# Kernel tuning notes

Measured on AMD Instinct MI355X. Metric: run time of the kernel, lower is better.

The kernel has to match this reference:

```python
import jax, jax.numpy as jnp
import numpy as np

TOP_K = 8
N_GROUPS = 8
TOP_K_GROUPS = 4
ROUTE_SCALE = 2.5


def setup_inputs() -> dict:
    key = jax.random.key(0)
    k1, k2, k3 = jax.random.split(key, 3)
    x = jax.random.normal(k1, (8192, 7168), dtype=jnp.float32)
    weight = jax.random.normal(k2, (256, 7168), dtype=jnp.float32) * 0.02
    bias = jax.random.normal(k3, (256,), dtype=jnp.float32) * 0.1
    return {"x": x, "weight": weight, "bias": bias}


def reference(x, weight, bias):
    n_tokens = x.shape[0]
    n_experts = weight.shape[0]
    # scores: [T, E]
    logits = jnp.einsum('td,ed->te', x, weight)
    scores = jax.nn.sigmoid(logits)
    original_scores = scores
    scores_b = scores + bias  # bias branch (dim == 7168)
    # group-limited routing
    sg = scores_b.reshape(n_tokens, N_GROUPS, n_experts // N_GROUPS)
    # bias is not None -> group score = sum of top-2 within group
    top2, _ = jax.lax.top_k(sg, 2)
    group_scores = top2.sum(axis=-1)  # [T, G]
    _, group_idx = jax.lax.top_k(group_scores, TOP_K_GROUPS)  # [T, Kg]
    keep = jnp.zeros((n_tokens, N_GROUPS), dtype=bool)
    keep = keep.at[jnp.arange(n_tokens)[:, None], group_idx].set(True)
    masked = jnp.where(keep[:, :, None], sg, -jnp.inf).reshape(n_tokens, n_experts)
    # global top-k over masked scores
    _, indices = jax.lax.top_k(masked, TOP_K)  # [T, K]
    weights = jnp.take_along_axis(original_scores, indices, axis=1)
    weights = weights / weights.sum(axis=-1, keepdims=True)  # sigmoid normalization
    weights = weights * ROUTE_SCALE
    return weights.astype(x.dtype), indices
```

## Files before the change

### kernel.cpp

```cpp
#include <hip/hip_runtime.h>
#include <math.h>

#define T_TOKENS 8192
#define NEXP 256
#define DIM 7168
#define NEG_INF (-3.0e38f)

typedef _Float16 f16;
typedef _Float16 f16x8 __attribute__((ext_vector_type(8)));
typedef __fp16 h16x2 __attribute__((ext_vector_type(2)));
typedef float f32x4 __attribute__((ext_vector_type(4)));

#define AS1 __attribute__((address_space(1)))
#define AS3 __attribute__((address_space(3)))

#define WTILED_BYTES (2 * NEXP * DIM * 2)
#define PART_OFF WTILED_BYTES
#define UNSCALE 5.9604644775390625e-8f

__global__ __launch_bounds__(256) void wconvert(const float* __restrict__ w,
                                                char* __restrict__ wt) {
    const int n = blockIdx.x * 256 + threadIdx.x;
    const int K8 = n % 896;
    const int e = n / 896;
    const f32x4 u0 = *(const f32x4*)(w + (size_t)e * DIM + K8 * 8);
    const f32x4 u1 = *(const f32x4*)(w + (size_t)e * DIM + K8 * 8 + 4);
    float c[8] = {u0[0]*4096.f, u0[1]*4096.f, u0[2]*4096.f, u0[3]*4096.f,
                  u1[0]*4096.f, u1[1]*4096.f, u1[2]*4096.f, u1[3]*4096.f};
    f16x8 h, g;
#pragma unroll
    for (int j = 0; j < 4; ++j) {
        h16x2 hp = __builtin_amdgcn_cvt_pkrtz(c[2*j], c[2*j+1]);
        float r0 = c[2*j]   - (float)hp[0];
        float r1 = c[2*j+1] - (float)hp[1];
        h16x2 gp = __builtin_amdgcn_cvt_pkrtz(r0, r1);
        h[2*j] = (f16)hp[0]; h[2*j+1] = (f16)hp[1];
        g[2*j] = (f16)gp[0]; g[2*j+1] = (f16)gp[1];
    }
    const int T = K8 >> 2, q = K8 & 3;
    const int bnq = e >> 6, nt = (e >> 4) & 3, l = e & 15;
    char* base = wt + ((size_t)(T * 4 + bnq)) * 8192 + q * 256 + l * 16;
    *(f16x8*)(base + (0 * 4 + nt) * 1024) = h;
    *(f16x8*)(base + (1 * 4 + nt) * 1024) = g;
}

__global__ __launch_bounds__(512) void gemm8w(
    const float* __restrict__ x, const char* __restrict__ wt,
    float* __restrict__ part, int ksplit) {
    __shared__ char smem[65536];
    const int tid = threadIdx.x;
    const int lane = tid & 63;
    const int wv = tid >> 6;
    const int bn = blockIdx.x, bm = blockIdx.y, bz = blockIdx.z;
    const int wr = wv >> 2, wcn = wv & 3;
    const int l15 = lane & 15, q4 = lane >> 4;
    const int niter = ksplit >> 5;

    const char* xc = (const char*)x;

    int aoff[2], ldsA[2];
#pragma unroll
    for (int i = 0; i < 2; ++i) {
        const int u = wv * 2 + i;
        const int ra = u * 8 + (lane >> 3);
        const int ua = lane & 7;
        aoff[i] = (bm * 128 + ra) * (DIM * 4) + bz * (ksplit * 4)
                + ((ua ^ (ra & 7)) * 16);
        ldsA[i] = u * 1024;
    }
    const char* wbase0 = wt + ((size_t)(bz * niter * 4 + bn * 2)) * 8192;
    int woff[2], ldsW[2];
#pragma unroll
    for (int i = 0; i < 2; ++i) {
        const int u = wv * 2 + i;
        woff[i] = u * 1024 + lane * 16;
        ldsW[i] = 16384 + u * 1024;
    }

    int rA[4][2];
#pragma unroll
    for (int m = 0; m < 4; ++m) {
        const int r = wr * 64 + m * 16 + l15;
        rA[m][0] = r * 128 + (((2 * q4 + 0) ^ (r & 7)) * 16);
        rA[m][1] = r * 128 + (((2 * q4 + 1) ^ (r & 7)) * 16);
    }
    int rW[2][2];
#pragma unroll
    for (int ntl = 0; ntl < 2; ++ntl)
#pragma unroll
        for (int p = 0; p < 2; ++p)
            rW[ntl][p] = 16384 + (wcn >> 1) * 8192
                       + (p * 4 + (wcn & 1) * 2 + ntl) * 1024 + q4 * 256 + l15 * 16;

    f32x4 acc[4][2];
#pragma unroll
    for (int m = 0; m < 4; ++m)
#pragma unroll
        for (int ntl = 0; ntl < 2; ++ntl) acc[m][ntl] = (f32x4){0.f, 0.f, 0.f, 0.f};

#define STAGE(sb)                                                               \
    {                                                                           \
        _Pragma("unroll")                                                       \
        for (int i = 0; i < 2; ++i)                                             \
            __builtin_amdgcn_global_load_lds((const AS1 void*)(xc + aoff[i]),   \
                (AS3 void*)(smem + (sb) + ldsA[i]), 16, 0, 0);                  \
        _Pragma("unroll")                                                       \
        for (int i = 0; i < 2; ++i)                                             \
            __builtin_amdgcn_global_load_lds((const AS1 void*)(wbase0 + woff[i]),\
                (AS3 void*)(smem + (sb) + ldsW[i]), 16, 0, 0);                  \
        _Pragma("unroll")                                                       \
        for (int i = 0; i < 2; ++i) { aoff[i] += 128; woff[i] += 32768; }       \
    }

#define COMPUTE(sb)                                                             \
    {                                                                           \
        f16x8 wb[2][2];                                                         \
        _Pragma("unroll")                                                       \
        for (int ntl = 0; ntl < 2; ++ntl) {                                     \
            wb[ntl][0] = *(const f16x8*)(smem + (sb) + rW[ntl][0]);             \
            wb[ntl][1] = *(const f16x8*)(smem + (sb) + rW[ntl][1]);             \
        }                                                                       \
        _Pragma("unroll")                                                       \
        for (int m = 0; m < 4; ++m) {                                           \
            const f32x4 v0 = *(const f32x4*)(smem + (sb) + rA[m][0]);           \
            const f32x4 v1 = *(const f32x4*)(smem + (sb) + rA[m][1]);           \
            float c[8] = {v0[0]*4096.f, v0[1]*4096.f, v0[2]*4096.f, v0[3]*4096.f,\
                          v1[0]*4096.f, v1[1]*4096.f, v1[2]*4096.f, v1[3]*4096.f};\
            f16x8 a0, a1;                                                       \
            _Pragma("unroll")                                                   \
            for (int j = 0; j < 4; ++j) {                                       \
                h16x2 hp = __builtin_amdgcn_cvt_pkrtz(c[2*j], c[2*j+1]);        \
                float r0 = c[2*j]   - (float)hp[0];                             \
                float r1 = c[2*j+1] - (float)hp[1];                             \
                h16x2 gp = __builtin_amdgcn_cvt_pkrtz(r0, r1);                  \
                a0[2*j] = (f16)hp[0]; a0[2*j+1] = (f16)hp[1];                   \
                a1[2*j] = (f16)gp[0]; a1[2*j+1] = (f16)gp[1];                   \
            }                                                                   \
            __builtin_amdgcn_s_setprio(1);                                      \
            _Pragma("unroll")                                                   \
            for (int ntl = 0; ntl < 2; ++ntl) {                                 \
                acc[m][ntl] = __builtin_amdgcn_mfma_f32_16x16x32_f16(a0, wb[ntl][0], acc[m][ntl], 0, 0, 0); \
                acc[m][ntl] = __builtin_amdgcn_mfma_f32_16x16x32_f16(a1, wb[ntl][0], acc[m][ntl], 0, 0, 0); \
                acc[m][ntl] = __builtin_amdgcn_mfma_f32_16x16x32_f16(a0, wb[ntl][1], acc[m][ntl], 0, 0, 0); \
                acc[m][ntl] = __builtin_amdgcn_mfma_f32_16x16x32_f16(a1, wb[ntl][1], acc[m][ntl], 0, 0, 0); \
            }                                                                   \
            __builtin_amdgcn_s_setprio(0);                                      \
        }                                                                       \
    }

    STAGE(0);
    for (int t = 0; t < niter - 1; ++t) {
        const int cur = (t & 1) * 32768;
        const int nxt = ((t + 1) & 1) * 32768;
        STAGE(nxt);
        asm volatile("s_waitcnt vmcnt(4)" ::: "memory");
        __builtin_amdgcn_sched_barrier(0);
        __builtin_amdgcn_s_barrier();
        COMPUTE(cur);
        __builtin_amdgcn_s_barrier();
    }
    asm volatile("s_waitcnt vmcnt(0)" ::: "memory");
    __builtin_amdgcn_sched_barrier(0);
    __builtin_amdgcn_s_barrier();
    COMPUTE(((niter - 1) & 1) * 32768);
#undef STAGE
#undef COMPUTE

    float* P = part + (size_t)bz * T_TOKENS * NEXP;
    const int orow = bm * 128 + wr * 64 + q4 * 4;
#pragma unroll
    for (int m = 0; m < 4; ++m)
#pragma unroll
        for (int ntl = 0; ntl < 2; ++ntl) {
            const int ocol = bn * 128 + wcn * 32 + ntl * 16 + l15;
#pragma unroll
            for (int r = 0; r < 4; ++r)
                P[(size_t)(orow + m * 16 + r) * NEXP + ocol] = acc[m][ntl][r];
        }
}

__global__ __launch_bounds__(256) void routing_kernel(const float* __restrict__ part,
                                                      const float* __restrict__ bias,
                                                      float* __restrict__ out, int nsplit) {
    const int lane = threadIdx.x & 63;
    const int t = blockIdx.x * 4 + (threadIdx.x >> 6);

    f32x4 z = {0.f, 0.f, 0.f, 0.f};
    for (int s = 0; s < nsplit; ++s) {
        const f32x4 v = *((const f32x4*)(part + ((size_t)s * T_TOKENS + t) * NEXP) + lane);
        z[0] += v[0]; z[1] += v[1]; z[2] += v[2]; z[3] += v[3];
    }
    const float s0 = 1.0f / (1.0f + expf(-z[0] * UNSCALE));
    const float s1 = 1.0f / (1.0f + expf(-z[1] * UNSCALE));
    const float s2 = 1.0f / (1.0f + expf(-z[2] * UNSCALE));
    const float s3 = 1.0f / (1.0f + expf(-z[3] * UNSCALE));
    const f32x4 bv = *((const f32x4*)bias + lane);
    float sb0 = s0 + bv[0], sb1 = s1 + bv[1], sb2 = s2 + bv[2], sb3 = s3 + bv[3];

    float m1, m2;
    m1 = sb0; m2 = NEG_INF;
    if (sb1 > m1) { m2 = m1; m1 = sb1; } else if (sb1 > m2) m2 = sb1;
    if (sb2 > m1) { m2 = m1; m1 = sb2; } else if (sb2 > m2) m2 = sb2;
    if (sb3 > m1) { m2 = m1; m1 = sb3; } else if (sb3 > m2) m2 = sb3;
#pragma unroll
    for (int off = 1; off < 8; off <<= 1) {
        const float om1 = __shfl_xor(m1, off);
        const float om2 = __shfl_xor(m2, off);
        const float hi = fmaxf(m1, om1);
        const float lo = fminf(m1, om1);
        m2 = fmaxf(lo, fmaxf(m2, om2));
        m1 = hi;
    }
    const float gs = m1 + m2;

    const float g0 = __shfl(gs, 0),  g1 = __shfl(gs, 8),  g2 = __shfl(gs, 16), g3 = __shfl(gs, 24);
    const float g4 = __shfl(gs, 32), g5 = __shfl(gs, 40), g6 = __shfl(gs, 48), g7 = __shfl(gs, 56);

    float t1 = NEG_INF, t2 = NEG_INF, t3 = NEG_INF, t4 = NEG_INF;
    int i1 = 0, i2 = 0, i3 = 0, i4 = 0;
#define INS4(v, gi)                                                         \
    {                                                                       \
        if (v > t1)      { t4=t3;i4=i3; t3=t2;i3=i2; t2=t1;i2=i1; t1=v;i1=gi; } \
        else if (v > t2) { t4=t3;i4=i3; t3=t2;i3=i2; t2=v;i2=gi; }          \
        else if (v > t3) { t4=t3;i4=i3; t3=v;i3=gi; }                       \
        else if (v > t4) { t4=v;i4=gi; }                                    \
    }
    INS4(g0, 0) INS4(g1, 1) INS4(g2, 2) INS4(g3, 3)
    INS4(g4, 4) INS4(g5, 5) INS4(g6, 6) INS4(g7, 7)
#undef INS4
    const int keepmask = (1 << i1) | (1 << i2) | (1 << i3) | (1 << i4);

    const int g = lane >> 3;
    if (!((keepmask >> g) & 1)) { sb0 = NEG_INF; sb1 = NEG_INF; sb2 = NEG_INF; sb3 = NEG_INF; }

    float wval[8];
    int wi[8];
    float wsum = 0.0f;
#pragma unroll
    for (int r = 0; r < 8; r++) {
        float bvv = sb0;
        int bii = (lane << 2);
        if (sb1 > bvv) { bvv = sb1; bii = (lane << 2) | 1; }
        if (sb2 > bvv) { bvv = sb2; bii = (lane << 2) | 2; }
        if (sb3 > bvv) { bvv = sb3; bii = (lane << 2) | 3; }
#pragma unroll
        for (int off = 1; off < 64; off <<= 1) {
            const float ov = __shfl_xor(bvv, off);
            const int oi = __shfl_xor(bii, off);
            if (ov > bvv || (ov == bvv && oi < bii)) { bvv = ov; bii = oi; }
        }
        const int sl = bii & 3;
        const float cand = (sl == 0) ? s0 : (sl == 1) ? s1 : (sl == 2) ? s2 : s3;
        const float ow = __shfl(cand, bii >> 2);
        wval[r] = ow;
        wi[r] = bii;
        wsum += ow;
        if ((bii >> 2) == lane) {
            if (sl == 0) sb0 = NEG_INF;
            else if (sl == 1) sb1 = NEG_INF;
            else if (sl == 2) sb2 = NEG_INF;
            else sb3 = NEG_INF;
        }
    }
    const float scale = 2.5f / wsum;
    if (lane == 0) {
        float* ow8 = out + (size_t)t * 8;
        float* oi8 = out + (size_t)T_TOKENS * 8 + (size_t)t * 8;
#pragma unroll
        for (int r = 0; r < 8; r++) {
            ow8[r] = wval[r] * scale;
            oi8[r] = (float)wi[r];
        }
    }
}

extern "C" void kernel_launch(void* const* d_in, const int* in_sizes, int n_in,
                              void* d_out, int out_size, void* d_ws, size_t ws_size,
                              hipStream_t stream) {
    const float* x = (const float*)d_in[0];
    const float* w = (const float*)d_in[1];
    const float* bias = (const float*)d_in[2];

    char* wt = (char*)d_ws;
    float* part = (float*)((char*)d_ws + PART_OFF);

    const size_t need4 = (size_t)PART_OFF + 4ull * T_TOKENS * NEXP * 4;
    const int nsplit = (ws_size >= need4) ? 4 : 2;
    const int ksplit = DIM / nsplit;

    wconvert<<<NEXP * DIM / (256 * 8), 256, 0, stream>>>(w, wt);
    gemm8w<<<dim3(2, 64, nsplit), 512, 0, stream>>>(x, wt, part, ksplit);
    routing_kernel<<<T_TOKENS / 4, 256, 0, stream>>>(part, bias, (float*)d_out, nsplit);
}
```

Baseline: 154.5 us.

## Compute full 256-expert tile per block with 32x32 MFMA and triple-buffered LDS

```diff
diff --git a/kernel.cpp b/kernel.cpp
--- a/kernel.cpp
+++ b/kernel.cpp
@@ -4,12 +4,16 @@
 #define T_TOKENS 8192
 #define NEXP 256
 #define DIM 7168
+#define NSPLIT 4
+#define KSPL (DIM / NSPLIT)
+#define NITER (KSPL / 32)
 #define NEG_INF (-3.0e38f)
 
 typedef _Float16 f16;
 typedef _Float16 f16x8 __attribute__((ext_vector_type(8)));
 typedef __fp16 h16x2 __attribute__((ext_vector_type(2)));
 typedef float f32x4 __attribute__((ext_vector_type(4)));
+typedef float f32x16 __attribute__((ext_vector_type(16)));
 
 #define AS1 __attribute__((address_space(1)))
 #define AS3 __attribute__((address_space(3)))
@@ -17,6 +21,7 @@
 #define WTILED_BYTES (2 * NEXP * DIM * 2)
 #define PART_OFF WTILED_BYTES
 #define UNSCALE 5.9604644775390625e-8f
+#define STG 49152
 
 __global__ __launch_bounds__(256) void wconvert(const float* __restrict__ w,
                                                 char* __restrict__ wt) {
@@ -37,24 +42,25 @@
         h[2*j] = (f16)hp[0]; h[2*j+1] = (f16)hp[1];
         g[2*j] = (f16)gp[0]; g[2*j+1] = (f16)gp[1];
     }
-    const int T = K8 >> 2, q = K8 & 3;
-    const int bnq = e >> 6, nt = (e >> 4) & 3, l = e & 15;
-    char* base = wt + ((size_t)(T * 4 + bnq)) * 8192 + q * 256 + l * 16;
-    *(f16x8*)(base + (0 * 4 + nt) * 1024) = h;
-    *(f16x8*)(base + (1 * 4 + nt) * 1024) = g;
+    const int T = K8 >> 2;
+    const int kk = (K8 >> 1) & 1;
+    const int lhi = K8 & 1;
+    const int ntg = e >> 5, l31 = e & 31;
+    char* base = wt + (size_t)T * 32768 + ntg * 1024 + lhi * 512 + l31 * 16;
+    *(f16x8*)(base + (kk * 2 + 0) * 8192) = h;
+    *(f16x8*)(base + (kk * 2 + 1) * 8192) = g;
 }
 
-__global__ __launch_bounds__(512) void gemm8w(
+__global__ __launch_bounds__(512, 2) void gemm32x(
     const float* __restrict__ x, const char* __restrict__ wt,
-    float* __restrict__ part, int ksplit) {
-    __shared__ char smem[65536];
+    float* __restrict__ part) {
+    extern __shared__ __align__(16) char smem[];
     const int tid = threadIdx.x;
     const int lane = tid & 63;
     const int wv = tid >> 6;
-    const int bn = blockIdx.x, bm = blockIdx.y, bz = blockIdx.z;
+    const int bm = blockIdx.x, bz = blockIdx.y;
     const int wr = wv >> 2, wcn = wv & 3;
-    const int l15 = lane & 15, q4 = lane >> 4;
-    const int niter = ksplit >> 5;
+    const int l31 = lane & 31, lhi = lane >> 5;
 
     const char* xc = (const char*)x;
 
@@ -64,39 +70,48 @@
         const int u = wv * 2 + i;
         const int ra = u * 8 + (lane >> 3);
         const int ua = lane & 7;
-        aoff[i] = (bm * 128 + ra) * (DIM * 4) + bz * (ksplit * 4)
+        aoff[i] = (bm * 128 + ra) * (DIM * 4) + bz * (KSPL * 4)
                 + ((ua ^ (ra & 7)) * 16);
         ldsA[i] = u * 1024;
     }
-    const char* wbase0 = wt + ((size_t)(bz * niter * 4 + bn * 2)) * 8192;
-    int woff[2], ldsW[2];
-#pragma unroll
-    for (int i = 0; i < 2; ++i) {
-        const int u = wv * 2 + i;
+    const char* wbase = wt + (size_t)bz * NITER * 32768;
+    int woff[4], ldsW[4];
+#pragma unroll
+    for (int i = 0; i < 4; ++i) {
+        const int u = wv * 4 + i;
         woff[i] = u * 1024 + lane * 16;
         ldsW[i] = 16384 + u * 1024;
     }
 
-    int rA[4][2];
-#pragma unroll
-    for (int m = 0; m < 4; ++m) {
-        const int r = wr * 64 + m * 16 + l15;
-        rA[m][0] = r * 128 + (((2 * q4 + 0) ^ (r & 7)) * 16);
-        rA[m][1] = r * 128 + (((2 * q4 + 1) ^ (r & 7)) * 16);
-    }
-    int rW[2][2];
-#pragma unroll
-    for (int ntl = 0; ntl < 2; ++ntl)
+    int rA[2][2][2];
+#pragma unroll
+    for (int mt = 0; mt < 2; ++mt)
+#pragma unroll
+        for (int kk = 0; kk < 2; ++kk) {
+            const int row = wr * 64 + mt * 32 + l31;
+#pragma unroll
+            for (int i = 0; i < 2; ++i) {
+                const int u = kk * 4 + lhi * 2 + i;
+                rA[mt][kk][i] = row * 128 + ((u ^ (row & 7)) * 16);
+            }
+        }
+    int rW[2][2][2];
+#pragma unroll
+    for (int kk = 0; kk < 2; ++kk)
 #pragma unroll
         for (int p = 0; p < 2; ++p)
-            rW[ntl][p] = 16384 + (wcn >> 1) * 8192
-                       + (p * 4 + (wcn & 1) * 2 + ntl) * 1024 + q4 * 256 + l15 * 16;
-
-    f32x4 acc[4][2];
-#pragma unroll
-    for (int m = 0; m < 4; ++m)
-#pragma unroll
-        for (int ntl = 0; ntl < 2; ++ntl) acc[m][ntl] = (f32x4){0.f, 0.f, 0.f, 0.f};
+#pragma unroll
+            for (int ntl = 0; ntl < 2; ++ntl)
+                rW[kk][p][ntl] = 16384 + ((kk * 2 + p) * 8 + wcn * 2 + ntl) * 1024
+                               + lhi * 512 + l31 * 16;
+
+    f32x16 acc[2][2];
+#pragma unroll
+    for (int mt = 0; mt < 2; ++mt)
+#pragma unroll
+        for (int ntl = 0; ntl < 2; ++ntl)
+#pragma unroll
+            for (int r = 0; r < 16; ++r) acc[mt][ntl][r] = 0.0f;
 
 #define STAGE(sb)                                                               \
     {                                                                           \
@@ -105,88 +120,108 @@
             __builtin_amdgcn_global_load_lds((const AS1 void*)(xc + aoff[i]),   \
                 (AS3 void*)(smem + (sb) + ldsA[i]), 16, 0, 0);                  \
         _Pragma("unroll")                                                       \
-        for (int i = 0; i < 2; ++i)                                             \
-            __builtin_amdgcn_global_load_lds((const AS1 void*)(wbase0 + woff[i]),\
+        for (int i = 0; i < 4; ++i)                                             \
+            __builtin_amdgcn_global_load_lds((const AS1 void*)(wbase + woff[i]),\
                 (AS3 void*)(smem + (sb) + ldsW[i]), 16, 0, 0);                  \
         _Pragma("unroll")                                                       \
-        for (int i = 0; i < 2; ++i) { aoff[i] += 128; woff[i] += 32768; }       \
-    }
-
-#define COMPUTE(sb)                                                             \
+        for (int i = 0; i < 2; ++i) aoff[i] += 128;                             \
+        _Pragma("unroll")                                                       \
+        for (int i = 0; i < 4; ++i) woff[i] += 32768;                           \
+    }
+
+#define COMPUTE(cb)                                                             \
     {                                                                           \
-        f16x8 wb[2][2];                                                         \
-        _Pragma("unroll")                                                       \
-        for (int ntl = 0; ntl < 2; ++ntl) {                                     \
-            wb[ntl][0] = *(const f16x8*)(smem + (sb) + rW[ntl][0]);             \
-            wb[ntl][1] = *(const f16x8*)(smem + (sb) + rW[ntl][1]);             \
-        }                                                                       \
-        _Pragma("unroll")                                                       \
-        for (int m = 0; m < 4; ++m) {                                           \
-            const f32x4 v0 = *(const f32x4*)(smem + (sb) + rA[m][0]);           \
-            const f32x4 v1 = *(const f32x4*)(smem + (sb) + rA[m][1]);           \
-            float c[8] = {v0[0]*4096.f, v0[1]*4096.f, v0[2]*4096.f, v0[3]*4096.f,\
-                          v1[0]*4096.f, v1[1]*4096.f, v1[2]*4096.f, v1[3]*4096.f};\
-            f16x8 a0, a1;                                                       \
+        _Pragma("unroll")                                                       \
+        for (int kk = 0; kk < 2; ++kk) {                                        \
+            f16x8 wb[2][2];                                                     \
             _Pragma("unroll")                                                   \
-            for (int j = 0; j < 4; ++j) {                                       \
-                h16x2 hp = __builtin_amdgcn_cvt_pkrtz(c[2*j], c[2*j+1]);        \
-                float r0 = c[2*j]   - (float)hp[0];                             \
-                float r1 = c[2*j+1] - (float)hp[1];                             \
-                h16x2 gp = __builtin_amdgcn_cvt_pkrtz(r0, r1);                  \
-                a0[2*j] = (f16)hp[0]; a0[2*j+1] = (f16)hp[1];                   \
-                a1[2*j] = (f16)gp[0]; a1[2*j+1] = (f16)gp[1];                   \
+            for (int p = 0; p < 2; ++p)                                         \
+                _Pragma("unroll")                                               \
+                for (int ntl = 0; ntl < 2; ++ntl)                               \
+                    wb[p][ntl] = *(const f16x8*)(smem + (cb) + rW[kk][p][ntl]); \
+            f16x8 a0[2], a1[2];                                                 \
+            _Pragma("unroll")                                                   \
+            for (int mt = 0; mt < 2; ++mt) {                                    \
+                const f32x4 v0 = *(const f32x4*)(smem + (cb) + rA[mt][kk][0]);  \
+                const f32x4 v1 = *(const f32x4*)(smem + (cb) + rA[mt][kk][1]);  \
+                float c[8] = {v0[0]*4096.f, v0[1]*4096.f, v0[2]*4096.f, v0[3]*4096.f,\
+                              v1[0]*4096.f, v1[1]*4096.f, v1[2]*4096.f, v1[3]*4096.f};\
+                _Pragma("unroll")                                               \
+                for (int j = 0; j < 4; ++j) {                                   \
+                    h16x2 hp = __builtin_amdgcn_cvt_pkrtz(c[2*j], c[2*j+1]);    \
+                    float r0 = c[2*j]   - (float)hp[0];                         \
+                    float r1 = c[2*j+1] - (float)hp[1];                         \
+                    h16x2 gp = __builtin_amdgcn_cvt_pkrtz(r0, r1);              \
+                    a0[mt][2*j] = (f16)hp[0]; a0[mt][2*j+1] = (f16)hp[1];       \
+                    a1[mt][2*j] = (f16)gp[0]; a1[mt][2*j+1] = (f16)gp[1];       \
+                }                                                               \
             }                                                                   \
             __builtin_amdgcn_s_setprio(1);                                      \
             _Pragma("unroll")                                                   \
-            for (int ntl = 0; ntl < 2; ++ntl) {                                 \
-                acc[m][ntl] = __builtin_amdgcn_mfma_f32_16x16x32_f16(a0, wb[ntl][0], acc[m][ntl], 0, 0, 0); \
-                acc[m][ntl] = __builtin_amdgcn_mfma_f32_16x16x32_f16(a1, wb[ntl][0], acc[m][ntl], 0, 0, 0); \
-                acc[m][ntl] = __builtin_amdgcn_mfma_f32_16x16x32_f16(a0, wb[ntl][1], acc[m][ntl], 0, 0, 0); \
-                acc[m][ntl] = __builtin_amdgcn_mfma_f32_16x16x32_f16(a1, wb[ntl][1], acc[m][ntl], 0, 0, 0); \
-            }                                                                   \
+            for (int mt = 0; mt < 2; ++mt)                                      \
+                _Pragma("unroll")                                               \
+                for (int ntl = 0; ntl < 2; ++ntl) {                             \
+                    acc[mt][ntl] = __builtin_amdgcn_mfma_f32_32x32x16_f16(a0[mt], wb[0][ntl], acc[mt][ntl], 0, 0, 0); \
+                    acc[mt][ntl] = __builtin_amdgcn_mfma_f32_32x32x16_f16(a1[mt], wb[0][ntl], acc[mt][ntl], 0, 0, 0); \
+                    acc[mt][ntl] = __builtin_amdgcn_mfma_f32_32x32x16_f16(a0[mt], wb[1][ntl], acc[mt][ntl], 0, 0, 0); \
+                    acc[mt][ntl] = __builtin_amdgcn_mfma_f32_32x32x16_f16(a1[mt], wb[1][ntl], acc[mt][ntl], 0, 0, 0); \
+                }                                                               \
             __builtin_amdgcn_s_setprio(0);                                      \
         }                                                                       \
     }
 
     STAGE(0);
-    for (int t = 0; t < niter - 1; ++t) {
-        const int cur = (t & 1) * 32768;
-        const int nxt = ((t + 1) & 1) * 32768;
-        STAGE(nxt);
-        asm volatile("s_waitcnt vmcnt(4)" ::: "memory");
+    STAGE(STG);
+    int cb = 0;
+    int nb = 2 * STG;
+    for (int t = 0; t < NITER - 2; ++t) {
+        STAGE(nb);
+        asm volatile("s_waitcnt vmcnt(12)" ::: "memory");
         __builtin_amdgcn_sched_barrier(0);
         __builtin_amdgcn_s_barrier();
-        COMPUTE(cur);
+        COMPUTE(cb);
         __builtin_amdgcn_s_barrier();
-    }
+        const int ob = cb;
+        cb = (cb == 2 * STG) ? 0 : cb + STG;
+        nb = ob;
+    }
+    asm volatile("s_waitcnt vmcnt(6)" ::: "memory");
+    __builtin_amdgcn_sched_barrier(0);
+    __builtin_amdgcn_s_barrier();
+    COMPUTE(cb);
+    __builtin_amdgcn_s_barrier();
+    cb = (cb == 2 * STG) ? 0 : cb + STG;
     asm volatile("s_waitcnt vmcnt(0)" ::: "memory");
     __builtin_amdgcn_sched_barrier(0);
     __builtin_amdgcn_s_barrier();
-    COMPUTE(((niter - 1) & 1) * 32768);
+    COMPUTE(cb);
 #undef STAGE
 #undef COMPUTE
 
     float* P = part + (size_t)bz * T_TOKENS * NEXP;
-    const int orow = bm * 128 + wr * 64 + q4 * 4;
-#pragma unroll
-    for (int m = 0; m < 4; ++m)
+#pragma unroll
+    for (int mt = 0; mt < 2; ++mt)
 #pragma unroll
         for (int ntl = 0; ntl < 2; ++ntl) {
-            const int ocol = bn * 128 + wcn * 32 + ntl * 16 + l15;
-#pragma unroll
-            for (int r = 0; r < 4; ++r)
-                P[(size_t)(orow + m * 16 + r) * NEXP + ocol] = acc[m][ntl][r];
+            const int gcol = (wcn * 2 + ntl) * 32 + l31;
+#pragma unroll
+            for (int r = 0; r < 16; ++r) {
+                const int row32 = (r & 3) + 8 * (r >> 2) + 4 * lhi;
+                const int grow = bm * 128 + wr * 64 + mt * 32 + row32;
+                P[(size_t)grow * NEXP + gcol] = acc[mt][ntl][r];
+            }
         }
 }
 
 __global__ __launch_bounds__(256) void routing_kernel(const float* __restrict__ part,
                                                       const float* __restrict__ bias,
-                                                      float* __restrict__ out, int nsplit) {
+                                                      float* __restrict__ out) {
     const int lane = threadIdx.x & 63;
     const int t = blockIdx.x * 4 + (threadIdx.x >> 6);
 
     f32x4 z = {0.f, 0.f, 0.f, 0.f};
-    for (int s = 0; s < nsplit; ++s) {
+#pragma unroll
+    for (int s = 0; s < NSPLIT; ++s) {
         const f32x4 v = *((const f32x4*)(part + ((size_t)s * T_TOKENS + t) * NEXP) + lane);
         z[0] += v[0]; z[1] += v[1]; z[2] += v[2]; z[3] += v[3];
     }
@@ -284,11 +319,10 @@
     char* wt = (char*)d_ws;
     float* part = (float*)((char*)d_ws + PART_OFF);
 
-    const size_t need4 = (size_t)PART_OFF + 4ull * T_TOKENS * NEXP * 4;
-    const int nsplit = (ws_size >= need4) ? 4 : 2;
-    const int ksplit = DIM / nsplit;
+    (void)hipFuncSetAttribute((const void*)gemm32x,
+                              hipFuncAttributeMaxDynamicSharedMemorySize, 3 * STG);
 
     wconvert<<<NEXP * DIM / (256 * 8), 256, 0, stream>>>(w, wt);
-    gemm8w<<<dim3(2, 64, nsplit), 512, 0, stream>>>(x, wt, part, ksplit);
-    routing_kernel<<<T_TOKENS / 4, 256, 0, stream>>>(part, bias, (float*)d_out, nsplit);
+    gemm32x<<<dim3(64, NSPLIT), 512, 3 * STG, stream>>>(x, wt, part);
+    routing_kernel<<<T_TOKENS / 4, 256, 0, stream>>>(part, bias, (float*)d_out);
 }
```

After: 154.2 us. No clear change (-0.2%).
